# Optimization experiments

Hardware: AMD Instinct MI355X
Metric: run time of the kernel (lower is better)

## Reference

```python
import jax, jax.numpy as jnp
import numpy as np

B, N, D, L, NREPEAT = 32, 577, 384, 12, 4
H = 4 * D  # mlp hidden
EPS = 1e-6


def ln(x, w, b):
    mu = jnp.mean(x, axis=-1, keepdims=True)
    var = jnp.mean(jnp.square(x - mu), axis=-1, keepdims=True)
    return (x - mu) * jax.lax.rsqrt(var + EPS) * w + b


def setup_inputs() -> dict:
    key = jax.random.key(0)
    ks = jax.random.split(key, 16)
    s = 0.02
    return {
        "x": jax.random.normal(ks[0], (B, N, D), dtype=jnp.float32),
        "norm1_w": jnp.ones((L, D), jnp.float32),
        "norm1_b": jnp.zeros((L, D), jnp.float32),
        "qkv_w": jax.random.normal(ks[1], (L, 3 * D, D), jnp.float32) * s,
        "qkv_b": jnp.zeros((L, 3 * D), jnp.float32),
        "qn_w": jnp.ones((L, D), jnp.float32),
        "qn_b": jnp.zeros((L, D), jnp.float32),
        "kn_w": jnp.ones((L, D), jnp.float32),
        "kn_b": jnp.zeros((L, D), jnp.float32),
        "an_w": jnp.ones((L, D), jnp.float32),
        "an_b": jnp.zeros((L, D), jnp.float32),
        "proj_w": jax.random.normal(ks[2], (L, D, D), jnp.float32) * s,
        "proj_b": jnp.zeros((L, D), jnp.float32),
        "ls1": jnp.full((L, D), 1e-5, jnp.float32),
        "norm2_w": jnp.ones((L, D), jnp.float32),
        "norm2_b": jnp.zeros((L, D), jnp.float32),
        "fc1_w": jax.random.normal(ks[3], (L, H, D), jnp.float32) * s,
        "fc1_b": jnp.zeros((L, H), jnp.float32),
        "fc2_w": jax.random.normal(ks[4], (L, D, H), jnp.float32) * s,
        "fc2_b": jnp.zeros((L, D), jnp.float32),
        "ls2": jnp.full((L, D), 1e-5, jnp.float32),
    }


def _forward(x, norm1_w, norm1_b, qkv_w, qkv_b, qn_w, qn_b, kn_w, kn_b,
             an_w, an_b, proj_w, proj_b, ls1, norm2_w, norm2_b,
             fc1_w, fc1_b, fc2_w, fc2_b, ls2):
    scale = 1.0 / np.sqrt(D).astype(np.float32)
    x_prime = x
    history = []  # list of [B, 1, D] cls tokens, grows each repeat
    for _ in range(NREPEAT):
        new_cls = x[:, 0:1]
        x = jnp.concatenate([new_cls, x_prime[:, 1:]], axis=1)  # [B, N, D]
        mem = jnp.concatenate([x] + history, axis=1)            # [B, N+t, D]
        for l in range(L):
            res1 = x
            xn = ln(x, norm1_w[l], norm1_b[l])
            # manual qkv split: q from normed x, k/v from UNNORMED mem
            q = xn @ qkv_w[l, :D].T + qkv_b[l, :D]
            k = mem @ qkv_w[l, D:2 * D].T + qkv_b[l, D:2 * D]
            v = mem @ qkv_w[l, 2 * D:].T + qkv_b[l, 2 * D:]
            q = ln(q, qn_w[l], qn_b[l])
            k = ln(k, kn_w[l], kn_b[l])
            # single-head SDPA over full width D
            attn = jax.nn.softmax(jnp.einsum('bqd,bkd->bqk', q, k) * scale, axis=-1)
            prod = jnp.einsum('bqk,bkd->bqd', attn, v)
            prod = ln(prod, an_w[l], an_b[l])
            proj = prod @ proj_w[l].T + proj_b[l]
            x = proj * ls1[l] + res1
            res2 = x
            x2 = ln(x, norm2_w[l], norm2_b[l])
            h = jax.nn.gelu(x2 @ fc1_w[l].T + fc1_b[l], approximate=False)
            x1 = h @ fc2_w[l].T + fc2_b[l]
            x = x1 * ls2[l] + res2
        history.append(new_cls)
    return x


def reference(x, norm1_w, norm1_b, qkv_w, qkv_b, qn_w, qn_b, kn_w, kn_b,
              an_w, an_b, proj_w, proj_b, ls1, norm2_w, norm2_b,
              fc1_w, fc1_b, fc2_w, fc2_b, ls2):
    return _forward(x, norm1_w, norm1_b, qkv_w, qkv_b, qn_w, qn_b, kn_w, kn_b,
                    an_w, an_b, proj_w, proj_b, ls1, norm2_w, norm2_b,
                    fc1_w, fc1_b, fc2_w, fc2_b, ls2)
```

## Files before the change

kernel.cpp:

```cpp
#include <hip/hip_runtime.h>
#include <math.h>

#define BB 32
#define NN 577
#define DD 384
#define HD 1536
#define LL 12
#define MP 640
#define NRPT 4

typedef __attribute__((ext_vector_type(8))) short bf16x8;
typedef __attribute__((ext_vector_type(4))) float f32x4;

__device__ __forceinline__ unsigned short f2bf(float f){
  unsigned u = __builtin_bit_cast(unsigned, f);
  u += 0x7fffu + ((u >> 16) & 1u);
  return (unsigned short)(u >> 16);
}
__device__ __forceinline__ float bf2f(unsigned short s){
  unsigned u = ((unsigned)s) << 16;
  return __builtin_bit_cast(float, u);
}

__device__ __forceinline__ void async16(void* lds, const void* g){
  __builtin_amdgcn_global_load_lds(
      (const __attribute__((address_space(1))) unsigned int*)g,
      (__attribute__((address_space(3))) unsigned int*)lds, 16, 0, 0);
}

__global__ void prep_k(float* __restrict__ x, const float* __restrict__ xp,
                       float* __restrict__ cls_r, const float* __restrict__ cls_hist,
                       unsigned short* __restrict__ mem, int r){
  int i = blockIdx.x * 256 + threadIdx.x;
  if (i >= BB*MP*DD) return;
  int d = i % DD;
  int n = (i / DD) % MP;
  int b = i / (MP*DD);
  float v; bool wr = true;
  if (n == 0){ v = x[(size_t)b*NN*DD + d]; cls_r[b*DD + d] = v; }
  else if (n < NN){ v = xp[((size_t)b*NN + n)*DD + d]; x[((size_t)b*NN + n)*DD + d] = v; wr = (r==0); }
  else if (n < NN + r){ v = cls_hist[(size_t)(n-NN)*BB*DD + b*DD + d]; wr = (n == NN + r - 1); }
  else { v = 0.f; wr = (r==0); }
  if (wr) mem[i] = f2bf(v);
}

__global__ void cast_all_k(const float* __restrict__ qkvw, const float* __restrict__ pw,
                           const float* __restrict__ f1w, const float* __restrict__ f2w,
                           unsigned short* __restrict__ wbuf){
  int i = blockIdx.x * 256 + threadIdx.x;
  const int QKV = 3*DD*DD;
  const int PRJ = DD*DD;
  const int F1  = HD*DD;
  const int TOT = QKV + PRJ + 2*F1;
  if (i >= LL*TOT) return;
  int l = i / TOT, j = i % TOT;
  float v;
  if (j < QKV) v = qkvw[(size_t)l*QKV + j];
  else if (j < QKV+PRJ) v = pw[(size_t)l*PRJ + (j-QKV)];
  else if (j < QKV+PRJ+F1) v = f1w[(size_t)l*F1 + (j-QKV-PRJ)];
  else v = f2w[(size_t)l*F1 + (j-QKV-PRJ-F1)];
  wbuf[i] = f2bf(v);
}

template<typename T>
__global__ __launch_bounds__(256) void ln4_k(const T* __restrict__ in, const float* __restrict__ w,
                                             const float* __restrict__ bias, unsigned short* __restrict__ out,
                                             int nrows){
  int row = blockIdx.x*4 + (threadIdx.x >> 6);
  if (row >= nrows) return;
  int lane = threadIdx.x & 63;
  const T* p = in + (size_t)row*DD;
  float v[6];
  if constexpr (sizeof(T) == 4){
    const float* pf = (const float*)p;
    float4 a = *(const float4*)(pf + lane*4);
    float2 c = *(const float2*)(pf + 256 + lane*2);
    v[0]=a.x; v[1]=a.y; v[2]=a.z; v[3]=a.w; v[4]=c.x; v[5]=c.y;
  } else {
    const unsigned short* ps = (const unsigned short*)p;
    ushort4 a = *(const ushort4*)(ps + lane*4);
    ushort2 c = *(const ushort2*)(ps + 256 + lane*2);
    v[0]=bf2f(a.x); v[1]=bf2f(a.y); v[2]=bf2f(a.z); v[3]=bf2f(a.w);
    v[4]=bf2f(c.x); v[5]=bf2f(c.y);
  }
  float s = v[0]+v[1]+v[2]+v[3]+v[4]+v[5];
  #pragma unroll
  for (int o=32;o;o>>=1) s += __shfl_xor(s, o, 64);
  float mu = s * (1.f/DD);
  float q = 0.f;
  #pragma unroll
  for (int i=0;i<6;i++){ float t = v[i]-mu; q += t*t; }
  #pragma unroll
  for (int o=32;o;o>>=1) q += __shfl_xor(q, o, 64);
  float rs = rsqrtf(q*(1.f/DD) + 1e-6f);
  float4 w4 = *(const float4*)(w + lane*4);
  float2 w2 = *(const float2*)(w + 256 + lane*2);
  float4 b4 = *(const float4*)(bias + lane*4);
  float2 b2 = *(const float2*)(bias + 256 + lane*2);
  unsigned short* po = out + (size_t)row*DD;
  ushort4 o4;
  o4.x = f2bf((v[0]-mu)*rs*w4.x + b4.x);
  o4.y = f2bf((v[1]-mu)*rs*w4.y + b4.y);
  o4.z = f2bf((v[2]-mu)*rs*w4.z + b4.z);
  o4.w = f2bf((v[3]-mu)*rs*w4.w + b4.w);
  *(ushort4*)(po + lane*4) = o4;
  ushort2 o2;
  o2.x = f2bf((v[4]-mu)*rs*w2.x + b2.x);
  o2.y = f2bf((v[5]-mu)*rs*w2.y + b2.y);
  *(ushort2*)(po + 256 + lane*2) = o2;
}

__global__ __launch_bounds__(256) void fixup_k(
    const unsigned short* __restrict__ mem,
    const unsigned short* __restrict__ wq,
    const float* __restrict__ qkvb,
    const float* __restrict__ knw, const float* __restrict__ knb,
    unsigned short* __restrict__ kc,
    unsigned short* __restrict__ vc,
    int row2){
  int task = blockIdx.x*4 + (threadIdx.x >> 6);
  int lane = threadIdx.x & 63;
  int kind = task & 1;
  int rsel = (task >> 1) & 1;
  int b    = task >> 2;
  int row  = rsel ? row2 : 0;
  const unsigned short* mrow = mem + ((size_t)b*MP + row)*DD;
  const unsigned short* W = wq + (size_t)(kind+1)*DD*DD;
  const float* bias = qkvb + (kind+1)*DD;

  float acc[6] = {0,0,0,0,0,0};
  for (int i=0;i<48;i++){
    bf16x8 m8 = *(const bf16x8*)(mrow + i*8);
    float mf[8];
    #pragma unroll
    for (int j=0;j<8;j++) mf[j] = bf2f((unsigned short)m8[j]);
    #pragma unroll
    for (int c=0;c<6;c++){
      bf16x8 w8 = *(const bf16x8*)(W + (size_t)(lane + c*64)*DD + i*8);
      #pragma unroll
      for (int j=0;j<8;j++) acc[c] += mf[j]*bf2f((unsigned short)w8[j]);
    }
  }
  #pragma unroll
  for (int c=0;c<6;c++) acc[c] += bias[lane + c*64];

  if (kind == 0){
    float s1 = 0.f, s2 = 0.f;
    #pragma unroll
    for (int c=0;c<6;c++){ s1 += acc[c]; s2 += acc[c]*acc[c]; }
    #pragma unroll
    for (int o=32;o;o>>=1){ s1 += __shfl_xor(s1, o, 64); s2 += __shfl_xor(s2, o, 64); }
    float mu = s1*(1.f/DD);
    float var = s2*(1.f/DD) - mu*mu;
    float rs = rsqrtf(fmaxf(var, 0.f) + 1e-6f);
    unsigned short* out = kc + ((size_t)b*MP + row)*DD;
    #pragma unroll
    for (int c=0;c<6;c++){
      int col = lane + c*64;
      out[col] = f2bf((acc[c]-mu)*rs*knw[col] + knb[col]);
    }
  } else {
    #pragma unroll
    for (int c=0;c<6;c++){
      int d = lane + c*64;
      vc[((size_t)b*DD + d)*MP + row] = f2bf(acc[c]);
    }
  }
}

template<int EPI>
__global__ __launch_bounds__(256) void gemm128(
    const unsigned short* __restrict__ A, int lda, int arows, long sA,
    const unsigned short* __restrict__ B, int ldb, int brows, long sB,
    const float* __restrict__ bias,
    int K, int N,
    float* __restrict__ outF, unsigned short* __restrict__ outB,
    int ldo, int orows, long sO,
    const float* __restrict__ ls){

  __shared__ unsigned short a_sh[2][128*32];
  __shared__ unsigned short b_sh[2][128*32];

  int tid  = threadIdx.x;
  int wave = tid >> 6, lane = tid & 63;
  int lr = lane & 15, kg = lane >> 4;
  int wm = wave >> 1, wn = wave & 1;
  int z = blockIdx.z;
  int row0 = blockIdx.y * 128;
  int col0 = blockIdx.x * 128;

  const unsigned short* Ab = A + (size_t)z*sA;
  const unsigned short* Bb = B + (size_t)z*sB;

  f32x4 zf = {0.f,0.f,0.f,0.f};
  f32x4 acc[4][4];
  #pragma unroll
  for (int i=0;i<4;i++)
    #pragma unroll
    for (int j=0;j<4;j++) acc[i][j] = zf;

  int ra[2], rb[2], kc[2];
  #pragma unroll
  for (int it=0; it<2; it++){
    int c = tid + it*256;
    int r = row0 + (c>>2); if (r > arows-1) r = arows-1;
    ra[it] = r;
    r = col0 + (c>>2); if (r > brows-1) r = brows-1;
    rb[it] = r;
    kc[it] = (c&3)*8;
  }

  for (int k0 = 0; k0 < K; k0 += 64){
    #pragma unroll
    for (int p=0;p<2;p++){
      #pragma unroll
      for (int it=0; it<2; it++){
        unsigned short* la = &a_sh[p][(it*256 + wave*64)*8];
        unsigned short* lb = &b_sh[p][(it*256 + wave*64)*8];
        async16(la, Ab + (size_t)ra[it]*lda + k0 + p*32 + kc[it]);
        async16(lb, Bb + (size_t)rb[it]*ldb + k0 + p*32 + kc[it]);
      }
    }
    __syncthreads();
    #pragma unroll
    for (int p=0;p<2;p++){
      bf16x8 af[4], bfr[4];
      #pragma unroll
      for (int i=0;i<4;i++){
        af[i]  = *(const bf16x8*)&a_sh[p][(wm*64 + i*16 + lr)*32 + kg*8];
        bfr[i] = *(const bf16x8*)&b_sh[p][(wn*64 + i*16 + lr)*32 + kg*8];
      }
      #pragma unroll
      for (int i=0;i<4;i++)
        #pragma unroll
        for (int j=0;j<4;j++)
          acc[i][j] = __builtin_amdgcn_mfma_f32_16x16x32_bf16(af[i], bfr[j], acc[i][j], 0,0,0);
    }
    __syncthreads();
  }

  float* oF = outF ? outF + (size_t)z*sO : nullptr;
  unsigned short* oB = outB ? outB + (size_t)z*sO : nullptr;

  #pragma unroll
  for (int mi=0;mi<4;mi++)
    #pragma unroll
    for (int ni=0;ni<4;ni++)
      #pragma unroll
      for (int r=0;r<4;r++){
        int row = row0 + wm*64 + mi*16 + kg*4 + r;
        int col = col0 + wn*64 + ni*16 + lr;
        if (row >= orows || col >= N) continue;
        float vv = acc[mi][ni][r];
        size_t idx = (size_t)row*ldo + col;
        if (EPI == 0){
          if (bias) vv += bias[col];
          oB[idx] = f2bf(vv);
        } else if (EPI == 1){
          vv += bias[row];
          oB[idx] = f2bf(vv);
        } else if (EPI == 2){
          vv += bias[col];
          oF[idx] = vv*ls[col] + oF[idx];
        } else {
          vv += bias[col];
          float g = 0.5f*vv*(1.f + erff(vv*0.70710678118f));
          oB[idx] = f2bf(g);
        }
      }
}

__global__ __launch_bounds__(256, 2) void attn_k(
    const unsigned short* __restrict__ qraw,
    const float* __restrict__ qw, const float* __restrict__ qb_,
    const unsigned short* __restrict__ kb,
    const unsigned short* __restrict__ vT,
    const float* __restrict__ anw, const float* __restrict__ anb,
    unsigned short* __restrict__ out, int M){

  __shared__ unsigned short k_sh[32*384];
  __shared__ unsigned short v_sh[384*32];
  __shared__ unsigned short p_sh[64*56];

  int tid = threadIdx.x;
  int wv = tid >> 6, lane = tid & 63;
  int lr = lane & 15, kg = lane >> 4;
  int b = blockIdx.y, qt0 = blockIdx.x * 64;

  bf16x8 qf[12];
  {
    int qrow = qt0 + wv*16 + lr; if (qrow > NN-1) qrow = NN-1;
    const unsigned short* qp = qraw + ((size_t)b*NN + qrow)*DD;
    float s1 = 0.f, s2 = 0.f;
    #pragma unroll
    for (int ks=0; ks<12; ks++){
      qf[ks] = *(const bf16x8*)(qp + ks*32 + kg*8);
      #pragma unroll
      for (int j=0;j<8;j++){
        float t = bf2f((unsigned short)qf[ks][j]);
        s1 += t; s2 += t*t;
      }
    }
    s1 += __shfl_xor(s1, 16, 64); s1 += __shfl_xor(s1, 32, 64);
    s2 += __shfl_xor(s2, 16, 64); s2 += __shfl_xor(s2, 32, 64);
    const float SC = 0.05103103588f;
    float mu = s1 * (1.f/DD);
    float var = s2 * (1.f/DD) - mu*mu;
    float rs = rsqrtf(fmaxf(var, 0.f) + 1e-6f) * SC;
    #pragma unroll
    for (int ks=0; ks<12; ks++){
      int c0 = ks*32 + kg*8;
      float4 wa = *(const float4*)(qw + c0);
      float4 wb = *(const float4*)(qw + c0 + 4);
      float4 ba = *(const float4*)(qb_ + c0);
      float4 bb = *(const float4*)(qb_ + c0 + 4);
      bf16x8 t;
      t[0] = (short)f2bf((bf2f((unsigned short)qf[ks][0])-mu)*rs*wa.x + ba.x*SC);
      t[1] = (short)f2bf((bf2f((unsigned short)qf[ks][1])-mu)*rs*wa.y + ba.y*SC);
      t[2] = (short)f2bf((bf2f((unsigned short)qf[ks][2])-mu)*rs*wa.z + ba.z*SC);
      t[3] = (short)f2bf((bf2f((unsigned short)qf[ks][3])-mu)*rs*wa.w + ba.w*SC);
      t[4] = (short)f2bf((bf2f((unsigned short)qf[ks][4])-mu)*rs*wb.x + bb.x*SC);
      t[5] = (short)f2bf((bf2f((unsigned short)qf[ks][5])-mu)*rs*wb.y + bb.y*SC);
      t[6] = (short)f2bf((bf2f((unsigned short)qf[ks][6])-mu)*rs*wb.z + bb.z*SC);
      t[7] = (short)f2bf((bf2f((unsigned short)qf[ks][7])-mu)*rs*wb.w + bb.w*SC);
      qf[ks] = t;
    }
  }

  f32x4 zf = {0.f,0.f,0.f,0.f};
  f32x4 O[24];
  #pragma unroll
  for (int i=0;i<24;i++) O[i] = zf;
  float m_run[4], l_run[4];
  #pragma unroll
  for (int r=0;r<4;r++){ m_run[r] = -INFINITY; l_run[r] = 0.f; }

  for (int kt=0; kt<19; kt++){
    __syncthreads();
    #pragma unroll
    for (int i=0;i<6;i++){
      int L = i*256 + tid;
      int row = L/48, c = L%48;
      int gc = (c & ~7) | ((c ^ row) & 7);
      async16(&k_sh[L*8], kb + ((size_t)b*MP + kt*32 + row)*DD + gc*8);
    }
    #pragma unroll
    for (int i=0;i<6;i++){
      int L = i*256 + tid;
      int row = L>>2;
      int gc = (L&3) ^ (row&3);
      async16(&v_sh[L*8], vT + ((size_t)b*DD + row)*MP + kt*32 + gc*8);
    }
    __syncthreads();

    f32x4 s[2] = {zf, zf};
    __builtin_amdgcn_s_setprio(1);
    #pragma unroll
    for (int ks=0; ks<12; ks++){
      int c = ks*4 + kg;
      #pragma unroll
      for (int nk=0; nk<2; nk++){
        int krow = nk*16 + lr;
        bf16x8 bk = *(const bf16x8*)&k_sh[krow*DD + ((c & ~7) | ((c ^ krow)&7))*8];
        s[nk] = __builtin_amdgcn_mfma_f32_16x16x32_bf16(qf[ks], bk, s[nk], 0,0,0);
      }
    }
    __builtin_amdgcn_s_setprio(0);
    #pragma unroll
    for (int nk=0; nk<2; nk++){
      if (kt*32 + nk*16 + lr >= M){
        s[nk][0] = -INFINITY; s[nk][1] = -INFINITY; s[nk][2] = -INFINITY; s[nk][3] = -INFINITY;
      }
    }
    float vmax[4];
    #pragma unroll
    for (int r=0;r<4;r++){
      float v = fmaxf(s[0][r], s[1][r]);
      v = fmaxf(v, __shfl_xor(v, 1, 64));
      v = fmaxf(v, __shfl_xor(v, 2, 64));
      v = fmaxf(v, __shfl_xor(v, 4, 64));
      v = fmaxf(v, __shfl_xor(v, 8, 64));
      vmax[r] = v;
    }
    bool small = (vmax[0] <= m_run[0] + 8.f) & (vmax[1] <= m_run[1] + 8.f)
               & (vmax[2] <= m_run[2] + 8.f) & (vmax[3] <= m_run[3] + 8.f);
    if (!__all(small)){
      #pragma unroll
      for (int r=0;r<4;r++){
        float mn = fmaxf(m_run[r], vmax[r]);
        float al = __expf(m_run[r] - mn);
        m_run[r] = mn;
        l_run[r] *= al;
        #pragma unroll
        for (int ni=0;ni<24;ni++) O[ni][r] *= al;
      }
    }
    #pragma unroll
    for (int nk=0;nk<2;nk++)
      #pragma unroll
      for (int r=0;r<4;r++)
        s[nk][r] = __expf(s[nk][r] - m_run[r]);
    #pragma unroll
    for (int r=0;r<4;r++){
      float v = s[0][r] + s[1][r];
      v += __shfl_xor(v, 1, 64);
      v += __shfl_xor(v, 2, 64);
      v += __shfl_xor(v, 4, 64);
      v += __shfl_xor(v, 8, 64);
      l_run[r] += v;
    }
    #pragma unroll
    for (int nk=0;nk<2;nk++)
      #pragma unroll
      for (int r=0;r<4;r++)
        p_sh[(wv*16 + kg*4 + r)*56 + nk*16 + lr] = f2bf(s[nk][r]);
    __syncthreads();

    bf16x8 ap = *(const bf16x8*)&p_sh[(wv*16 + lr)*56 + kg*8];
    __builtin_amdgcn_s_setprio(1);
    #pragma unroll
    for (int ni=0;ni<24;ni++){
      int d = ni*16 + lr;
      bf16x8 bv = *(const bf16x8*)&v_sh[d*32 + ((kg ^ (d&3))*8)];
      O[ni] = __builtin_amdgcn_mfma_f32_16x16x32_bf16(ap, bv, O[ni], 0,0,0);
    }
    __builtin_amdgcn_s_setprio(0);
  }

  float inv[4];
  #pragma unroll
  for (int r=0;r<4;r++) inv[r] = 1.f / l_run[r];
  float s1[4] = {0,0,0,0}, s2[4] = {0,0,0,0};
  #pragma unroll
  for (int ni=0;ni<24;ni++)
    #pragma unroll
    for (int r=0;r<4;r++){
      float x = O[ni][r]*inv[r];
      O[ni][r] = x;
      s1[r] += x; s2[r] += x*x;
    }
  #pragma unroll
  for (int r=0;r<4;r++){
    #pragma unroll
    for (int o=1;o<16;o<<=1){ s1[r] += __shfl_xor(s1[r], o, 64); s2[r] += __shfl_xor(s2[r], o, 64); }
  }
  float mu[4], rs[4];
  #pragma unroll
  for (int r=0;r<4;r++){
    mu[r] = s1[r]*(1.f/DD);
    float var = s2[r]*(1.f/DD) - mu[r]*mu[r];
    rs[r] = rsqrtf(fmaxf(var, 0.f) + 1e-6f);
  }
  int rowb = qt0 + wv*16 + kg*4;
  #pragma unroll
  for (int ni=0;ni<24;ni++){
    int col = ni*16 + lr;
    float wc = anw[col], bc = anb[col];
    #pragma unroll
    for (int r=0;r<4;r++){
      int qrow = rowb + r;
      if (qrow < NN)
        out[((size_t)b*NN + qrow)*DD + col] = f2bf((O[ni][r]-mu[r])*rs[r]*wc + bc);
    }
  }
}


extern "C" void kernel_launch(void* const* d_in, const int* in_sizes, int n_in,
                              void* d_out, int out_size, void* d_ws, size_t ws_size,
                              hipStream_t stream){
  const float* x_in = (const float*)d_in[0];
  const float* n1w  = (const float*)d_in[1];
  const float* n1b  = (const float*)d_in[2];
  const float* qkvw = (const float*)d_in[3];
  const float* qkvb = (const float*)d_in[4];
  const float* qnw  = (const float*)d_in[5];
  const float* qnb  = (const float*)d_in[6];
  const float* knw  = (const float*)d_in[7];
  const float* knb  = (const float*)d_in[8];
  const float* anw  = (const float*)d_in[9];
  const float* anb  = (const float*)d_in[10];
  const float* pw   = (const float*)d_in[11];
  const float* pb   = (const float*)d_in[12];
  const float* ls1  = (const float*)d_in[13];
  const float* n2w  = (const float*)d_in[14];
  const float* n2b  = (const float*)d_in[15];
  const float* f1w  = (const float*)d_in[16];
  const float* f1b  = (const float*)d_in[17];
  const float* f2w  = (const float*)d_in[18];
  const float* f2bb = (const float*)d_in[19];
  const float* ls2  = (const float*)d_in[20];

  const int QKV = 3*DD*DD, PRJ = DD*DD, F1 = HD*DD;
  const size_t WTOT = (size_t)QKV + PRJ + 2*F1;
  const size_t SLOT = (size_t)BB*MP*DD;

  auto aln = [](size_t v){ return (v + 255) & ~(size_t)255; };
  const size_t WB = aln(LL*WTOT*2);
  const size_t CH = aln((size_t)NRPT*BB*DD*4);
  const size_t MB_ = aln(SLOT*2);
  const size_t SL = aln(SLOT*2);
  const size_t HB = aln((size_t)BB*NN*HD*2);
  const size_t CPL = 2*SL;

  char* ws = (char*)d_ws;
  size_t off = 0;
  auto take = [&](size_t bytes)->char* { char* p = ws + off; off += bytes; return p; };

  unsigned short* wbuf   = (unsigned short*)take(WB);
  float*          cls_h  = (float*)         take(CH);
  unsigned short* mem_bf = (unsigned short*)take(MB_);
  unsigned short* S0     = (unsigned short*)take(SL);
  unsigned short* HQ     = (unsigned short*)take(HB);

  int nc;
  unsigned short *kscr = nullptr, *vscr = nullptr, *kcache = nullptr, *vcache = nullptr;
  if (off + (size_t)LL*CPL <= ws_size){
    nc = LL;
    kcache = (unsigned short*)take((size_t)LL*SL);
    vcache = (unsigned short*)take((size_t)LL*SL);
  } else {
    kscr = (unsigned short*)take(SL);
    vscr = (unsigned short*)take(SL);
    size_t avail = (ws_size > off) ? ws_size - off : 0;
    nc = (int)(avail / CPL); if (nc > LL) nc = LL; if (nc < 0) nc = 0;
    kcache = (unsigned short*)take((size_t)nc*SL);
    vcache = (unsigned short*)take((size_t)nc*SL);
  }

  unsigned short* xn    = S0;
  unsigned short* qraw  = HQ;
  unsigned short* prodn = S0;
  unsigned short* x2    = S0;
  unsigned short* h     = HQ;

  float* xf = (float*)d_out;

  auto cg = [](size_t n){ return dim3((unsigned)((n + 255) / 256)); };

  hipMemcpyAsync(xf, x_in, (size_t)BB*NN*DD*4, hipMemcpyDeviceToDevice, stream);

  const int RT  = (BB*NN + 127)/128;
  const int RTM = (BB*MP)/128;
  const int QR  = BB*NN;
  const int KR  = BB*MP;

  cast_all_k<<<cg((size_t)LL*WTOT),256,0,stream>>>(qkvw, pw, f1w, f2w, wbuf);

  for (int r = 0; r < NRPT; r++){
    int M = NN + r;
    prep_k<<<cg((size_t)BB*MP*DD),256,0,stream>>>(xf, x_in, cls_h + (size_t)r*BB*DD, cls_h, mem_bf, r);
    for (int l = 0; l < LL; l++){
      const unsigned short* wl = wbuf + (size_t)l*WTOT;
      const unsigned short* wq = wl;
      const unsigned short* wp = wl + QKV;
      const unsigned short* w1 = wl + QKV + PRJ;
      const unsigned short* w2 = wl + QKV + PRJ + F1;

      bool cached = (l < nc);
      unsigned short* kbuf = cached ? kcache + (size_t)l*SLOT : kscr;
      unsigned short* vbuf = cached ? vcache + (size_t)l*SLOT : vscr;

      ln4_k<float><<<cg((size_t)QR*64),256,0,stream>>>(xf, n1w + l*DD, n1b + l*DD, xn, QR);
      gemm128<0><<<dim3(3,RT,1),256,0,stream>>>(xn,384,QR,0, wq,384,384,0,
          qkvb + l*3*DD, 384,384, nullptr,qraw,384,QR,0, nullptr);

      if (!cached || r == 0){
        gemm128<0><<<dim3(3,RTM,1),256,0,stream>>>(mem_bf,384,KR,0, wq + (size_t)DD*DD,384,384,0,
            qkvb + l*3*DD + DD, 384,384, nullptr,kbuf,384,KR,0, nullptr);
        gemm128<1><<<dim3(MP/128,3,BB),256,0,stream>>>(wq + (size_t)2*DD*DD,384,384,0, mem_bf,384,MP,(long)MP*DD,
            qkvb + l*3*DD + 2*DD, 384,MP, nullptr,vbuf,MP,384,(long)DD*MP, nullptr);
        ln4_k<unsigned short><<<cg((size_t)KR*64),256,0,stream>>>(kbuf, knw + l*DD, knb + l*DD, kbuf, KR);
      } else {
        fixup_k<<<32,256,0,stream>>>(mem_bf, wq, qkvb + l*3*DD,
                                     knw + l*DD, knb + l*DD, kbuf, vbuf, NN + r - 1);
      }

      attn_k<<<dim3(10,BB),256,0,stream>>>(qraw, qnw + l*DD, qnb + l*DD, kbuf, vbuf,
                                           anw + l*DD, anb + l*DD, prodn, M);
      gemm128<2><<<dim3(3,RT,1),256,0,stream>>>(prodn,384,QR,0, wp,384,384,0,
          pb + l*DD, 384,384, xf,nullptr,384,QR,0, ls1 + l*DD);
      ln4_k<float><<<cg((size_t)QR*64),256,0,stream>>>(xf, n2w + l*DD, n2b + l*DD, x2, QR);
      gemm128<3><<<dim3(HD/128,RT,1),256,0,stream>>>(x2,384,QR,0, w1,384,HD,0,
          f1b + l*HD, 384,HD, nullptr,h,HD,QR,0, nullptr);
      gemm128<2><<<dim3(3,RT,1),256,0,stream>>>(h,HD,QR,0, w2,HD,384,0,
          f2bb + l*DD, HD,384, xf,nullptr,384,QR,0, ls2 + l*DD);
    }
  }
}
```

Measured before the change: 16.84 ms.

## Double-buffer LDS tiles in gemm128 to overlap global loads with MFMA

```diff
diff --git a/kernel.cpp b/kernel.cpp
--- a/kernel.cpp
+++ b/kernel.cpp
@@ -169,7 +169,7 @@
 }
 
 template<int EPI>
-__global__ __launch_bounds__(256) void gemm128(
+__global__ __launch_bounds__(256, 2) void gemm128(
     const unsigned short* __restrict__ A, int lda, int arows, long sA,
     const unsigned short* __restrict__ B, int ldb, int brows, long sB,
     const float* __restrict__ bias,
@@ -178,8 +178,8 @@
     int ldo, int orows, long sO,
     const float* __restrict__ ls){
 
-  __shared__ unsigned short a_sh[2][128*32];
-  __shared__ unsigned short b_sh[2][128*32];
+  __shared__ unsigned short a_sh[2][2][128*32];
+  __shared__ unsigned short b_sh[2][2][128*32];
 
   int tid  = threadIdx.x;
   int wave = tid >> 6, lane = tid & 63;
@@ -210,25 +210,33 @@
     kc[it] = (c&3)*8;
   }
 
-  for (int k0 = 0; k0 < K; k0 += 64){
+  auto stage = [&](int buf, int k0){
     #pragma unroll
     for (int p=0;p<2;p++){
       #pragma unroll
       for (int it=0; it<2; it++){
-        unsigned short* la = &a_sh[p][(it*256 + wave*64)*8];
-        unsigned short* lb = &b_sh[p][(it*256 + wave*64)*8];
-        async16(la, Ab + (size_t)ra[it]*lda + k0 + p*32 + kc[it]);
-        async16(lb, Bb + (size_t)rb[it]*ldb + k0 + p*32 + kc[it]);
-      }
-    }
-    __syncthreads();
+        async16(&a_sh[buf][p][(it*256 + wave*64)*8], Ab + (size_t)ra[it]*lda + k0 + p*32 + kc[it]);
+        async16(&b_sh[buf][p][(it*256 + wave*64)*8], Bb + (size_t)rb[it]*ldb + k0 + p*32 + kc[it]);
+      }
+    }
+  };
+
+  int nt = K >> 6;
+  stage(0, 0);
+  asm volatile("s_waitcnt vmcnt(0)" ::: "memory");
+  __builtin_amdgcn_s_barrier();
+
+  for (int t=0; t<nt; t++){
+    int cur = t & 1;
+    if (t+1 < nt) stage(cur^1, (t+1)*64);
+    __builtin_amdgcn_s_setprio(1);
     #pragma unroll
     for (int p=0;p<2;p++){
       bf16x8 af[4], bfr[4];
       #pragma unroll
       for (int i=0;i<4;i++){
-        af[i]  = *(const bf16x8*)&a_sh[p][(wm*64 + i*16 + lr)*32 + kg*8];
-        bfr[i] = *(const bf16x8*)&b_sh[p][(wn*64 + i*16 + lr)*32 + kg*8];
+        af[i]  = *(const bf16x8*)&a_sh[cur][p][(wm*64 + i*16 + lr)*32 + kg*8];
+        bfr[i] = *(const bf16x8*)&b_sh[cur][p][(wn*64 + i*16 + lr)*32 + kg*8];
       }
       #pragma unroll
       for (int i=0;i<4;i++)
@@ -236,7 +244,9 @@
         for (int j=0;j<4;j++)
           acc[i][j] = __builtin_amdgcn_mfma_f32_16x16x32_bf16(af[i], bfr[j], acc[i][j], 0,0,0);
     }
-    __syncthreads();
+    __builtin_amdgcn_s_setprio(0);
+    asm volatile("s_waitcnt vmcnt(0)" ::: "memory");
+    __builtin_amdgcn_s_barrier();
   }
 
   float* oF = outF ? outF + (size_t)z*sO : nullptr;
```

Result: slower. 17.35 ms (+3.0%).
